# Optimization experiments

Measured on AMD Instinct MI355X. Metric: run time of the kernel, lower is better.

The kernel has to match this reference:

```python
import jax, jax.numpy as jnp
import numpy as np

B, L = 32, 512
D_EMB = 500      # tagger_mlp_layer
LANG = 100       # tagger_embeddings_size
H = 800          # tagger_encoder_size * 2
P_ARC = 100      # parser_arc_proj_size
P_LAB = 400      # parser_label_proj_size
MLP = 500        # tagger_mlp_layer (aux_mlp out)
N_LANG, N_LAB, N_UPOS, N_XPOS, N_ATTRS = 8, 50, 20, 300, 500


def setup_inputs() -> dict:
    key = jax.random.key(0)
    ks = jax.random.split(key, 24)
    s = 0.05
    lang_table = jax.random.normal(ks[3], (N_LANG, LANG), jnp.float32) * s
    lang_table = lang_table.at[0].set(0.0)  # padding_idx=0
    return {
        "emb": jax.random.normal(ks[0], (B, L, D_EMB), jnp.float32),
        "hidden": jax.random.normal(ks[1], (B, L, H), jnp.float32),
        "lang_ids": jax.random.randint(ks[2], (B,), 0, N_LANG),
        "lang_table": lang_table,
        "W_arc": jax.random.normal(ks[4], (P_ARC, D_EMB + LANG), jnp.float32) * s,
        "b_arc": jax.random.normal(ks[5], (P_ARC,), jnp.float32) * s,
        "W_lab": jax.random.normal(ks[6], (P_LAB, D_EMB + LANG), jnp.float32) * s,
        "b_lab": jax.random.normal(ks[7], (P_LAB,), jnp.float32) * s,
        "w_head": jax.random.normal(ks[8], (2 * P_ARC,), jnp.float32) * s,
        "b_head": jax.random.normal(ks[9], (1,), jnp.float32) * s,
        "W_aux": jax.random.normal(ks[10], (MLP, H), jnp.float32) * s,
        "b_aux": jax.random.normal(ks[11], (MLP,), jnp.float32) * s,
        "W_upos": jax.random.normal(ks[12], (N_UPOS, MLP + LANG), jnp.float32) * s,
        "b_upos": jax.random.normal(ks[13], (N_UPOS,), jnp.float32) * s,
        "W_xpos": jax.random.normal(ks[14], (N_XPOS, MLP + LANG), jnp.float32) * s,
        "b_xpos": jax.random.normal(ks[15], (N_XPOS,), jnp.float32) * s,
        "W_attrs": jax.random.normal(ks[16], (N_ATTRS, MLP + LANG), jnp.float32) * s,
        "b_attrs": jax.random.normal(ks[17], (N_ATTRS,), jnp.float32) * s,
    }


def reference(emb, hidden, lang_ids, lang_table, W_arc, b_arc, W_lab, b_lab,
              w_head, b_head, W_aux, b_aux, W_upos, b_upos, W_xpos, b_xpos,
              W_attrs, b_attrs):
    Bv, Lv = emb.shape[0], emb.shape[1]
    lang_emb = lang_table[lang_ids]                              # [B, LANG]
    lang_rep = jnp.broadcast_to(lang_emb[:, None, :], (Bv, Lv, lang_emb.shape[-1]))
    ho = jnp.concatenate((emb, lang_rep), axis=2)                # [B, L, D_EMB+LANG]

    proj_arc = jnp.tanh(jnp.einsum('bld,pd->blp', ho, W_arc) + b_arc)   # [B, L, P_ARC]
    proj_label = jnp.tanh(jnp.einsum('bld,pd->blp', ho, W_lab) + b_lab) # [B, L, P_LAB]

    # Biaffine decomposition of output_head(cat(pa[i], pa[j])):
    # score(i,j) = pa[i] . w1 + pa[j] . w2 + b
    P = proj_arc.shape[-1]
    s1 = proj_arc @ w_head[:P]                                   # [B, L]
    s2 = proj_arc @ w_head[P:]                                   # [B, L]
    core = s1[:, :, None] + s2[:, None, :] + b_head[0]           # [B, L, L]
    arcs = jnp.concatenate(
        (jnp.zeros((Bv, Lv, 1), core.dtype), core), axis=2)     # [B, L, L+1]

    aux_hid = jnp.tanh(jnp.einsum('blh,mh->blm', hidden, W_aux) + b_aux)  # [B, L, MLP]
    aux_cat = jnp.concatenate((aux_hid, lang_rep), axis=2)
    s_upos = jnp.einsum('blm,um->blu', aux_cat, W_upos) + b_upos
    s_xpos = jnp.einsum('blm,um->blu', aux_cat, W_xpos) + b_xpos
    s_attrs = jnp.einsum('blm,um->blu', aux_cat, W_attrs) + b_attrs
    return arcs, proj_label, s_upos, s_xpos, s_attrs
```

## Files before the change

kernel.cpp:

```cpp
#include <hip/hip_runtime.h>


using f16   = _Float16;
using f16x4 = __attribute__((ext_vector_type(4))) _Float16;
using f16x8 = __attribute__((ext_vector_type(8))) _Float16;
using f32x4 = __attribute__((ext_vector_type(4))) float;

__device__ __forceinline__ f16 f2h(float f) { return (f16)f; }
__device__ __forceinline__ f16x4 cvt4(float4 v) {
  return f16x4{ f2h(v.x), f2h(v.y), f2h(v.z), f2h(v.w) };
}

__device__ __forceinline__ float fast_tanh(float x) {
  float xc = fminf(fmaxf(x, -15.f), 15.f);
  float e  = __builtin_amdgcn_exp2f(xc * 2.885390081777927f);
  return 1.f - 2.f * __builtin_amdgcn_rcpf(e + 1.f);
}

__device__ __forceinline__ void async16(void* lds, const void* gp) {
  __builtin_amdgcn_global_load_lds(
      (const __attribute__((address_space(1))) unsigned int*)gp,
      (__attribute__((address_space(3))) unsigned int*)lds, 16, 0, 0);
}

__global__ __launch_bounds__(256) void setup_kernel(
    const float* __restrict__ W_arc, const float* __restrict__ b_arc,
    const float* __restrict__ W_lab, const float* __restrict__ b_lab,
    const float* __restrict__ W_aux, const float* __restrict__ b_aux,
    const float* __restrict__ W_upos, const float* __restrict__ b_upos,
    const float* __restrict__ W_xpos, const float* __restrict__ b_xpos,
    const float* __restrict__ W_attrs, const float* __restrict__ b_attrs,
    f16* __restrict__ W_proj, f16* __restrict__ W_auxp, f16* __restrict__ W_heads,
    float* __restrict__ bias_proj, float* __restrict__ bias_aux, float* __restrict__ bias_heads)
{
  const int blk = blockIdx.x, t = threadIdx.x;
  if (blk < 1376) {
    int w = blk * 256 + t;
    const float* src = nullptr;
    f16* dst;
    if (w < 81920) {
      int n = w / 160, s = w - n * 160;
      dst = W_proj + (size_t)w * 4;
      if (s < 150 && n < 500)
        src = (n < 100 ? W_arc + (size_t)n * 600
                       : W_lab + (size_t)(n - 100) * 600) + s * 4;
    } else if (w < 81920 + 106496) {
      int w2 = w - 81920;
      int n = w2 / 208, s = w2 - n * 208;
      dst = W_auxp + (size_t)w2 * 4;
      if (s < 200 && n < 500) src = W_aux + (size_t)n * 800 + s * 4;
    } else {
      int w3 = w - (81920 + 106496);
      int n = w3 / 160, s = w3 - n * 160;
      dst = W_heads + (size_t)w3 * 4;
      if (s < 150 && n < 820)
        src = (n < 20 ? W_upos + (size_t)n * 600
              : n < 320 ? W_xpos + (size_t)(n - 20) * 600
                        : W_attrs + (size_t)(n - 320) * 600) + s * 4;
    }
    f16x4 h = { (f16)0.f, (f16)0.f, (f16)0.f, (f16)0.f };
    if (src) h = cvt4(*(const float4*)src);
    *(f16x4*)dst = h;
    return;
  }
  for (int idx = t; idx < 2048; idx += 256) {
    if (idx < 512) {
      float v = 0.f;
      if (idx < 100)      v = b_arc[idx];
      else if (idx < 500) v = b_lab[idx - 100];
      bias_proj[idx] = v;
    } else if (idx < 1024) {
      int i = idx - 512;
      bias_aux[i] = (i < 500) ? b_aux[i] : 0.f;
    } else {
      int i = idx - 1024; float v = 0.f;
      if (i < 20)       v = b_upos[i];
      else if (i < 320) v = b_xpos[i - 20];
      else if (i < 820) v = b_attrs[i - 320];
      bias_heads[i] = v;
    }
  }
}

__global__ __launch_bounds__(512, 2) void gemm01(
    const float* __restrict__ emb, const float* __restrict__ hidden,
    const float* __restrict__ lang_table, const int* __restrict__ lang_ids,
    const f16* __restrict__ W_proj, const f16* __restrict__ W_auxp,
    const float* __restrict__ bias_proj, const float* __restrict__ bias_aux,
    float* __restrict__ out_label, const float* __restrict__ w_head,
    float* __restrict__ s1, float* __restrict__ s2, f16* __restrict__ aux_cat)
{
  __shared__ __align__(16) f16 ldsA[2 * 16384];
  __shared__ __align__(16) f16 ldsB[2 * 16384];
  __shared__ float s1red[2][256], s2red[2][256];

  const int tid  = threadIdx.x;
  const int lane = tid & 63;
  const int wave = tid >> 6;
  const int wm = wave >> 2, wn = wave & 3;
  const int m16 = lane & 15, quad = lane >> 4;
  const int bm  = blockIdx.x;
  const int bny = blockIdx.y;
  const bool is0 = (bny < 2);
  const int bn  = is0 ? bny : bny - 2;
  const int K   = is0 ? 640 : 832;
  const int NT  = is0 ? 10 : 13;

  const int sr = lane >> 3;
  const int ssB = (lane & 7) ^ sr;
  const f16* Bmat = is0 ? W_proj : W_auxp;
  const f16* gB[4];
#pragma unroll
  for (int i = 0; i < 4; ++i)
    gB[i] = Bmat + (size_t)(bn * 256 + i * 64 + wave * 8 + sr) * K + ssB * 8;
  f16* sB = ldsB + wave * 512;

  const int ssA = lane & 7;
  const float* lrow = lang_table + (size_t)lang_ids[bm >> 1] * 100;
  const float* srcA[4];
  int dstA[4];
#pragma unroll
  for (int i = 0; i < 4; ++i) {
    const int rowA = wave * 32 + i * 8 + (lane >> 3);
    const int grow = bm * 256 + rowA;
    srcA[i] = is0 ? emb + (size_t)grow * 500 : hidden + (size_t)grow * 800;
    dstA[i] = rowA * 64 + ((ssA ^ (rowA & 7)) * 8);
  }
  float4 va[4], vb[4];

  const int aBase = (wm * 128 + m16) * 64;
  const int bBase = (wn * 64  + m16) * 64;
  const int sw0 = ((quad)     ^ (m16 & 7)) * 8;
  const int sw1 = ((4 | quad) ^ (m16 & 7)) * 8;

  f32x4 acc[8][4] = {};
  f16x8 af[4], bf[4];

#define ASTAGE(tt) do { const int k0b = (tt) * 64 + ssA * 8;                    \
    _Pragma("unroll")                                                           \
    for (int i2 = 0; i2 < 4; ++i2) {                                            \
      float4 x0 = {0.f,0.f,0.f,0.f}, x1 = {0.f,0.f,0.f,0.f};                    \
      if (is0) {                                                                \
        if (k0b < 500) { x0 = *(const float4*)(srcA[i2] + k0b);                 \
          x1 = (k0b + 4 < 500) ? *(const float4*)(srcA[i2] + k0b + 4)           \
                               : *(const float4*)(lrow); }                      \
        else if (k0b < 600) { x0 = *(const float4*)(lrow + k0b - 500);          \
                              x1 = *(const float4*)(lrow + k0b - 496); }        \
      } else if (k0b < 800) { x0 = *(const float4*)(srcA[i2] + k0b);            \
                              x1 = *(const float4*)(srcA[i2] + k0b + 4); }      \
      va[i2] = x0; vb[i2] = x1; } } while (0)

#define AWRITE(nbf) do { _Pragma("unroll")                                      \
    for (int i2 = 0; i2 < 4; ++i2) {                                            \
      f16x8 hw = { f2h(va[i2].x), f2h(va[i2].y), f2h(va[i2].z), f2h(va[i2].w),  \
                   f2h(vb[i2].x), f2h(vb[i2].y), f2h(vb[i2].z), f2h(vb[i2].w) };\
      *(f16x8*)&ldsA[(nbf) + dstA[i2]] = hw; } } while (0)

#define BWISSUE(k0n, nbf) do {                                                  \
    async16(sB + (nbf) + 0 * 4096, gB[0] + (k0n));                              \
    async16(sB + (nbf) + 1 * 4096, gB[1] + (k0n));                              \
    async16(sB + (nbf) + 2 * 4096, gB[2] + (k0n));                              \
    async16(sB + (nbf) + 3 * 4096, gB[3] + (k0n)); } while (0)

#define RDA(mqv, sw) { _Pragma("unroll")                                        \
  for (int ii = 0; ii < 4; ++ii)                                                \
    af[ii] = *(const f16x8*)&ldsA[buf + aBase + (mqv) * 4096 + ii * 1024 + (sw)]; }
#define RDB(sw) { _Pragma("unroll")                                             \
  for (int j = 0; j < 4; ++j)                                                   \
    bf[j] = *(const f16x8*)&ldsB[buf + bBase + j * 1024 + (sw)]; }
#define MM(mqv) { _Pragma("unroll")                                             \
  for (int ii = 0; ii < 4; ++ii) { _Pragma("unroll")                            \
    for (int j = 0; j < 4; ++j)                                                 \
      acc[(mqv) * 4 + ii][j] = __builtin_amdgcn_mfma_f32_16x16x32_f16(          \
          af[ii], bf[j], acc[(mqv) * 4 + ii][j], 0, 0, 0); } }
#define SBAR __builtin_amdgcn_sched_barrier(0)
#define VM4  asm volatile("s_waitcnt vmcnt(4)" ::: "memory")
#define VM0  asm volatile("s_waitcnt vmcnt(0)" ::: "memory")
#define LGK0 asm volatile("s_waitcnt lgkmcnt(0)" ::: "memory")
#define BAR  __builtin_amdgcn_s_barrier()
#define PRIO1 __builtin_amdgcn_s_setprio(1)
#define PRIO0 __builtin_amdgcn_s_setprio(0)

  ASTAGE(0);
  SBAR;
  BWISSUE(0, 0);
  SBAR; VM4; SBAR;
  AWRITE(0);
  VM0;
  LGK0;
  BAR;

  for (int t = 0; t < NT; ++t) {
    const int buf = (t & 1) << 14;
    const int nbf = ((t + 1) & 1) << 14;
    const bool st = (t + 1 < NT);
    const int k0n = (t + 1) << 6;

    RDB(sw0); RDA(0, sw0);
    if (st) ASTAGE(t + 1);
    SBAR;
    if (st) BWISSUE(k0n, nbf);
    PRIO1; MM(0); PRIO0;
    RDA(1, sw0);
    PRIO1; MM(1); PRIO0;
    RDB(sw1); RDA(0, sw1);
    PRIO1; MM(0); PRIO0;
    RDA(1, sw1);
    PRIO1; MM(1); PRIO0;
    if (st) {
      SBAR; VM4; SBAR;
      AWRITE(nbf);
    }
    VM0;
    LGK0;
    BAR;
  }
#undef ASTAGE
#undef AWRITE
#undef BWISSUE
#undef RDA
#undef RDB
#undef MM
#undef SBAR
#undef VM4
#undef VM0
#undef LGK0
#undef BAR
#undef PRIO1
#undef PRIO0

  const int row0 = bm * 256 + wm * 128 + quad * 4;
  const int colT = bn * 256 + wn * 64 + m16;

  if (is0) {
    const float* bias = bias_proj;
    float p1[8][4] = {}, p2[8][4] = {};
    const bool haveHead = (bn == 0);
#pragma unroll
    for (int ai = 0; ai < 8; ++ai) {
#pragma unroll
      for (int j = 0; j < 4; ++j) {
        const int col = colT + j * 16;
        const float bcol = bias[col];
        float w1c = 0.f, w2c = 0.f;
        if (haveHead && col < 100) { w1c = w_head[col]; w2c = w_head[100 + col]; }
#pragma unroll
        for (int r = 0; r < 4; ++r) {
          const int row = row0 + ai * 16 + r;
          float v = fast_tanh(acc[ai][j][r] + bcol);
          if (col >= 100 && col < 500) out_label[(size_t)row * 400 + col - 100] = v;
          p1[ai][r] += v * w1c;
          p2[ai][r] += v * w2c;
        }
      }
    }
    if (haveHead) {
      if (wn < 2) {
#pragma unroll
        for (int d = 1; d < 16; d <<= 1)
#pragma unroll
          for (int ai = 0; ai < 8; ++ai)
#pragma unroll
            for (int r = 0; r < 4; ++r) {
              p1[ai][r] += __shfl_xor(p1[ai][r], d);
              p2[ai][r] += __shfl_xor(p2[ai][r], d);
            }
        if (m16 == 0) {
#pragma unroll
          for (int ai = 0; ai < 8; ++ai)
#pragma unroll
            for (int r = 0; r < 4; ++r) {
              int rl = wm * 128 + ai * 16 + quad * 4 + r;
              s1red[wn][rl] = p1[ai][r];
              s2red[wn][rl] = p2[ai][r];
            }
        }
      }
      __syncthreads();
      if (tid < 256) s1[bm * 256 + tid] = s1red[0][tid] + s1red[1][tid];
      else { int t2 = tid - 256; s2[bm * 256 + t2] = s2red[0][t2] + s2red[1][t2]; }
    }
  } else {
    const float* bias = bias_aux;
#pragma unroll
    for (int ai = 0; ai < 8; ++ai)
#pragma unroll
      for (int j = 0; j < 4; ++j) {
        const int col = colT + j * 16;
        if (col < 500) {
          const float bcol = bias[col];
#pragma unroll
          for (int r = 0; r < 4; ++r) {
            const int row = row0 + ai * 16 + r;
            aux_cat[(size_t)row * 640 + col] = f2h(fast_tanh(acc[ai][j][r] + bcol));
          }
        }
      }
    if (bn == 0) {
      for (int idx = tid; idx < 256 * 35; idx += 512) {
        int rr = idx / 35, qq = idx - rr * 35;
        int col = 500 + 4 * qq;
        f16x4 h = { (f16)0.f, (f16)0.f, (f16)0.f, (f16)0.f };
        if (col < 600) h = cvt4(*(const float4*)(lrow + col - 500));
        *(f16x4*)(aux_cat + (size_t)(bm * 256 + rr) * 640 + col) = h;
      }
    }
  }
}

__global__ __launch_bounds__(512, 2) void gemm2_arcs(
    const f16* __restrict__ aux_cat, const f16* __restrict__ W_heads,
    const float* __restrict__ bias_heads,
    const float* __restrict__ s1, const float* __restrict__ s2,
    const float* __restrict__ b_head,
    float* __restrict__ out_arcs, float* __restrict__ out_upos,
    float* __restrict__ out_xpos, float* __restrict__ out_attrs)
{
  __shared__ __align__(16) f16 ldsA[2 * 16384];
  __shared__ __align__(16) f16 ldsB[2 * 16384];

  const int tid  = threadIdx.x;
  const int lane = tid & 63;
  const int wave = tid >> 6;
  const int wm = wave >> 2, wn = wave & 3;
  const int m16 = lane & 15, quad = lane >> 4;
  const int bm = blockIdx.x, bn = blockIdx.y;
  const int K = 640, NT = 10;

  const int sr = lane >> 3;
  const int ss = (lane & 7) ^ sr;
  const f16* gA[4]; const f16* gB[4];
#pragma unroll
  for (int i = 0; i < 4; ++i) {
    gA[i] = aux_cat + (size_t)(bm * 256 + i * 64 + wave * 8 + sr) * K + ss * 8;
    gB[i] = W_heads + (size_t)(bn * 256 + i * 64 + wave * 8 + sr) * K + ss * 8;
  }
  f16* sA = ldsA + wave * 512;
  f16* sB = ldsB + wave * 512;

  const int aBase = (wm * 128 + m16) * 64;
  const int bBase = (wn * 64  + m16) * 64;
  const int sw0 = ((quad)     ^ (m16 & 7)) * 8;
  const int sw1 = ((4 | quad) ^ (m16 & 7)) * 8;

  f32x4 acc[8][4] = {};
  f16x8 af[4], bf[4];

#define STAGE8(k0n, nbf) do {                                                   \
    async16(sA + (nbf) + 0 * 4096, gA[0] + (k0n));                              \
    async16(sA + (nbf) + 1 * 4096, gA[1] + (k0n));                              \
    async16(sA + (nbf) + 2 * 4096, gA[2] + (k0n));                              \
    async16(sA + (nbf) + 3 * 4096, gA[3] + (k0n));                              \
    async16(sB + (nbf) + 0 * 4096, gB[0] + (k0n));                              \
    async16(sB + (nbf) + 1 * 4096, gB[1] + (k0n));                              \
    async16(sB + (nbf) + 2 * 4096, gB[2] + (k0n));                              \
    async16(sB + (nbf) + 3 * 4096, gB[3] + (k0n)); } while (0)

#define RDA(mqv, sw) { _Pragma("unroll")                                        \
  for (int ii = 0; ii < 4; ++ii)                                                \
    af[ii] = *(const f16x8*)&ldsA[buf + aBase + (mqv) * 4096 + ii * 1024 + (sw)]; }
#define RDB(sw) { _Pragma("unroll")                                             \
  for (int j = 0; j < 4; ++j)                                                   \
    bf[j] = *(const f16x8*)&ldsB[buf + bBase + j * 1024 + (sw)]; }
#define MM(mqv) { _Pragma("unroll")                                             \
  for (int ii = 0; ii < 4; ++ii) { _Pragma("unroll")                            \
    for (int j = 0; j < 4; ++j)                                                 \
      acc[(mqv) * 4 + ii][j] = __builtin_amdgcn_mfma_f32_16x16x32_f16(          \
          af[ii], bf[j], acc[(mqv) * 4 + ii][j], 0, 0, 0); } }
#define VM0  asm volatile("s_waitcnt vmcnt(0)" ::: "memory")
#define BAR  __builtin_amdgcn_s_barrier()
#define PRIO1 __builtin_amdgcn_s_setprio(1)
#define PRIO0 __builtin_amdgcn_s_setprio(0)

  STAGE8(0, 0);
  VM0;
  BAR;

  for (int t = 0; t < NT; ++t) {
    const int buf = (t & 1) << 14;
    const int nbf = ((t + 1) & 1) << 14;
    const bool st = (t + 1 < NT);
    const int k0n = (t + 1) << 6;

    RDB(sw0); RDA(0, sw0);
    if (st) STAGE8(k0n, nbf);
    PRIO1; MM(0); PRIO0;
    RDA(1, sw0);
    PRIO1; MM(1); PRIO0;
    RDB(sw1); RDA(0, sw1);
    PRIO1; MM(0); PRIO0;
    RDA(1, sw1);
    PRIO1; MM(1); PRIO0;
    VM0;
    BAR;
  }
#undef STAGE8
#undef RDA
#undef RDB
#undef MM
#undef VM0
#undef BAR
#undef PRIO1
#undef PRIO0

  const int row0 = bm * 256 + wm * 128 + quad * 4;
  const int colT = bn * 256 + wn * 64 + m16;
#pragma unroll
  for (int ai = 0; ai < 8; ++ai)
#pragma unroll
    for (int j = 0; j < 4; ++j) {
      const int col = colT + j * 16;
      const float bcol = bias_heads[col];
#pragma unroll
      for (int r = 0; r < 4; ++r) {
        const int row = row0 + ai * 16 + r;
        float v = acc[ai][j][r] + bcol;
        if (col < 20)        out_upos[(size_t)row * 20 + col] = v;
        else if (col < 320)  out_xpos[(size_t)row * 300 + col - 20] = v;
        else if (col < 820)  out_attrs[(size_t)row * 500 + col - 320] = v;
      }
    }

  const int r0 = bm * 256 + bn * 64;
  const float bh = b_head[0];
  const float s2v = s2[((r0 >> 9) << 9) + tid];
  for (int rl = 0; rl < 64; ++rl) {
    const int row = r0 + rl;
    const float s1v = s1[row] + bh;
    float* orow = out_arcs + (size_t)row * 513;
    if (tid == 0) orow[0] = 0.f;
    orow[1 + tid] = s1v + s2v;
  }
}

extern "C" void kernel_launch(void* const* d_in, const int* in_sizes, int n_in,
                              void* d_out, int out_size, void* d_ws, size_t ws_size,
                              hipStream_t stream)
{
  const float* emb      = (const float*)d_in[0];
  const float* hidden   = (const float*)d_in[1];
  const int*   lang_ids = (const int*)d_in[2];
  const float* lang_tab = (const float*)d_in[3];
  const float* W_arc  = (const float*)d_in[4];
  const float* b_arc  = (const float*)d_in[5];
  const float* W_lab  = (const float*)d_in[6];
  const float* b_lab  = (const float*)d_in[7];
  const float* w_head = (const float*)d_in[8];
  const float* b_head = (const float*)d_in[9];
  const float* W_aux  = (const float*)d_in[10];
  const float* b_aux  = (const float*)d_in[11];
  const float* W_upos = (const float*)d_in[12];
  const float* b_upos = (const float*)d_in[13];
  const float* W_xpos = (const float*)d_in[14];
  const float* b_xpos = (const float*)d_in[15];
  const float* W_attrs = (const float*)d_in[16];
  const float* b_attrs = (const float*)d_in[17];

  char* ws = (char*)d_ws;
  f16* aux_cat = (f16*)(ws + 0);
  f16* W_proj  = (f16*)(ws + 20971520);
  f16* W_auxp  = (f16*)(ws + 21626880);
  f16* W_heads = (f16*)(ws + 22478848);
  float* bias_proj  = (float*)(ws + 23789568);
  float* bias_aux   = (float*)(ws + 23791616);
  float* bias_heads = (float*)(ws + 23793664);
  float* s1         = (float*)(ws + 23797760);
  float* s2         = (float*)(ws + 23863296);

  float* out       = (float*)d_out;
  float* out_arcs  = out;
  float* out_label = out + 8404992;
  float* out_upos  = out + 14958592;
  float* out_xpos  = out + 15286272;
  float* out_attrs = out + 20201472;

  setup_kernel<<<1377, 256, 0, stream>>>(
      W_arc, b_arc, W_lab, b_lab, W_aux, b_aux,
      W_upos, b_upos, W_xpos, b_xpos, W_attrs, b_attrs,
      W_proj, W_auxp, W_heads, bias_proj, bias_aux, bias_heads);

  gemm01<<<dim3(64, 4), 512, 0, stream>>>(
      emb, hidden, lang_tab, lang_ids, W_proj, W_auxp, bias_proj, bias_aux,
      out_label, w_head, s1, s2, aux_cat);

  gemm2_arcs<<<dim3(64, 4), 512, 0, stream>>>(
      aux_cat, W_heads, bias_heads, s1, s2, b_head,
      out_arcs, out_upos, out_xpos, out_attrs);
}
```

Before: 267.2 us.

## Shrink GEMM tiles to 128x128x32 with 256-thread blocks and triple-buffered A

Both GEMM kernels move from 256x256 tiles with K-step 64 and 512 threads to 128x128 tiles with K-step 32 and 256 threads. This gives four times as many blocks (1024 instead of 256) to fill the 256 CUs, and uses a new LDS swizzle. The aux weight matrix is no longer padded to K=832, which drops the padded K iterations. gemm2 gains a three-stage A pipeline, and the arcs write is re-split across rows. In exchange, each block reuses less data, so more of A and B must be read from L2, and there are more barriers per unit of work.

```diff
diff --git a/kernel.cpp b/kernel.cpp
--- a/kernel.cpp
+++ b/kernel.cpp
@@ -34,7 +34,7 @@
     float* __restrict__ bias_proj, float* __restrict__ bias_aux, float* __restrict__ bias_heads)
 {
   const int blk = blockIdx.x, t = threadIdx.x;
-  if (blk < 1376) {
+  if (blk < 1360) {
     int w = blk * 256 + t;
     const float* src = nullptr;
     f16* dst;
@@ -44,13 +44,12 @@
       if (s < 150 && n < 500)
         src = (n < 100 ? W_arc + (size_t)n * 600
                        : W_lab + (size_t)(n - 100) * 600) + s * 4;
-    } else if (w < 81920 + 106496) {
+    } else if (w < 184320) {
       int w2 = w - 81920;
-      int n = w2 / 208, s = w2 - n * 208;
       dst = W_auxp + (size_t)w2 * 4;
-      if (s < 200 && n < 500) src = W_aux + (size_t)n * 800 + s * 4;
+      if (w2 < 100000) src = W_aux + (size_t)w2 * 4;
     } else {
-      int w3 = w - (81920 + 106496);
+      int w3 = w - 184320;
       int n = w3 / 160, s = w3 - n * 160;
       dst = W_heads + (size_t)w3 * 4;
       if (s < 150 && n < 820)
@@ -82,7 +81,7 @@
   }
 }
 
-__global__ __launch_bounds__(512, 2) void gemm01(
+__global__ __launch_bounds__(256, 4) void gemm01(
     const float* __restrict__ emb, const float* __restrict__ hidden,
     const float* __restrict__ lang_table, const int* __restrict__ lang_ids,
     const f16* __restrict__ W_proj, const f16* __restrict__ W_auxp,
@@ -90,55 +89,55 @@
     float* __restrict__ out_label, const float* __restrict__ w_head,
     float* __restrict__ s1, float* __restrict__ s2, f16* __restrict__ aux_cat)
 {
-  __shared__ __align__(16) f16 ldsA[2 * 16384];
-  __shared__ __align__(16) f16 ldsB[2 * 16384];
-  __shared__ float s1red[2][256], s2red[2][256];
+  __shared__ __align__(16) f16 ldsA[2 * 4096];
+  __shared__ __align__(16) f16 ldsB[2 * 4096];
+  __shared__ float s1red[2][128], s2red[2][128];
 
   const int tid  = threadIdx.x;
   const int lane = tid & 63;
   const int wave = tid >> 6;
-  const int wm = wave >> 2, wn = wave & 3;
+  const int wm = wave >> 1, wn = wave & 1;
   const int m16 = lane & 15, quad = lane >> 4;
   const int bm  = blockIdx.x;
   const int bny = blockIdx.y;
-  const bool is0 = (bny < 2);
-  const int bn  = is0 ? bny : bny - 2;
-  const int K   = is0 ? 640 : 832;
-  const int NT  = is0 ? 10 : 13;
-
-  const int sr = lane >> 3;
-  const int ssB = (lane & 7) ^ sr;
+  const bool is0 = (bny < 4);
+  const int bn  = is0 ? bny : bny - 4;
+  const int K   = is0 ? 640 : 800;
+  const int NT  = is0 ? 20 : 25;
+
+  const int sigR  = (m16 & 3) ^ ((m16 >> 2) & 3);
+  const int sigS  = ((lane >> 2) & 3) ^ quad;
+  const int kap   = lane & 3;
+
   const f16* Bmat = is0 ? W_proj : W_auxp;
-  const f16* gB[4];
-#pragma unroll
-  for (int i = 0; i < 4; ++i)
-    gB[i] = Bmat + (size_t)(bn * 256 + i * 64 + wave * 8 + sr) * K + ssB * 8;
-  f16* sB = ldsB + wave * 512;
-
-  const int ssA = lane & 7;
-  const float* lrow = lang_table + (size_t)lang_ids[bm >> 1] * 100;
-  const float* srcA[4];
-  int dstA[4];
-#pragma unroll
-  for (int i = 0; i < 4; ++i) {
-    const int rowA = wave * 32 + i * 8 + (lane >> 3);
-    const int grow = bm * 256 + rowA;
+  const int kapB = kap ^ sigS;
+  const f16* gB[2];
+#pragma unroll
+  for (int j = 0; j < 2; ++j)
+    gB[j] = Bmat + (size_t)(bn * 128 + wave * 32 + j * 16 + (lane >> 2)) * K + kapB * 8;
+  const int sBoff = wave * 1024;
+
+  const float* lrow = lang_table + (size_t)lang_ids[bm >> 2] * 100;
+  const float* srcA[2];
+  int dstA[2];
+#pragma unroll
+  for (int i = 0; i < 2; ++i) {
+    const int rowL = wave * 32 + i * 16 + (lane >> 2);
+    const int grow = bm * 128 + rowL;
     srcA[i] = is0 ? emb + (size_t)grow * 500 : hidden + (size_t)grow * 800;
-    dstA[i] = rowA * 64 + ((ssA ^ (rowA & 7)) * 8);
-  }
-  float4 va[4], vb[4];
-
-  const int aBase = (wm * 128 + m16) * 64;
-  const int bBase = (wn * 64  + m16) * 64;
-  const int sw0 = ((quad)     ^ (m16 & 7)) * 8;
-  const int sw1 = ((4 | quad) ^ (m16 & 7)) * 8;
-
-  f32x4 acc[8][4] = {};
+    dstA[i] = rowL * 32 + ((kap ^ sigS) * 8);
+  }
+  float4 va[2], vb[2];
+
+  const int baseA = (wm * 64 + m16) * 32 + ((quad ^ sigR) * 8);
+  const int baseB = (wn * 64 + m16) * 32 + ((quad ^ sigR) * 8);
+
+  f32x4 acc[4][4] = {};
   f16x8 af[4], bf[4];
 
-#define ASTAGE(tt) do { const int k0b = (tt) * 64 + ssA * 8;                    \
+#define ASTAGE(tt) do { const int k0b = (tt) * 32 + kap * 8;                    \
     _Pragma("unroll")                                                           \
-    for (int i2 = 0; i2 < 4; ++i2) {                                            \
+    for (int i2 = 0; i2 < 2; ++i2) {                                            \
       float4 x0 = {0.f,0.f,0.f,0.f}, x1 = {0.f,0.f,0.f,0.f};                    \
       if (is0) {                                                                \
         if (k0b < 500) { x0 = *(const float4*)(srcA[i2] + k0b);                 \
@@ -146,35 +145,33 @@
                                : *(const float4*)(lrow); }                      \
         else if (k0b < 600) { x0 = *(const float4*)(lrow + k0b - 500);          \
                               x1 = *(const float4*)(lrow + k0b - 496); }        \
-      } else if (k0b < 800) { x0 = *(const float4*)(srcA[i2] + k0b);            \
-                              x1 = *(const float4*)(srcA[i2] + k0b + 4); }      \
+      } else { x0 = *(const float4*)(srcA[i2] + k0b);                           \
+               x1 = *(const float4*)(srcA[i2] + k0b + 4); }                     \
       va[i2] = x0; vb[i2] = x1; } } while (0)
 
-#define AWRITE(nbf) do { _Pragma("unroll")                                      \
-    for (int i2 = 0; i2 < 4; ++i2) {                                            \
+#define AWRITE(nbfA) do { _Pragma("unroll")                                     \
+    for (int i2 = 0; i2 < 2; ++i2) {                                            \
       f16x8 hw = { f2h(va[i2].x), f2h(va[i2].y), f2h(va[i2].z), f2h(va[i2].w),  \
                    f2h(vb[i2].x), f2h(vb[i2].y), f2h(vb[i2].z), f2h(vb[i2].w) };\
-      *(f16x8*)&ldsA[(nbf) + dstA[i2]] = hw; } } while (0)
-
-#define BWISSUE(k0n, nbf) do {                                                  \
-    async16(sB + (nbf) + 0 * 4096, gB[0] + (k0n));                              \
-    async16(sB + (nbf) + 1 * 4096, gB[1] + (k0n));                              \
-    async16(sB + (nbf) + 2 * 4096, gB[2] + (k0n));                              \
-    async16(sB + (nbf) + 3 * 4096, gB[3] + (k0n)); } while (0)
-
-#define RDA(mqv, sw) { _Pragma("unroll")                                        \
+      *(f16x8*)&ldsA[(nbfA) + dstA[i2]] = hw; } } while (0)
+
+#define BWISSUE(tt, nbfB) do {                                                  \
+    async16(&ldsB[(nbfB) + sBoff],       gB[0] + (tt) * 32);                    \
+    async16(&ldsB[(nbfB) + sBoff + 512], gB[1] + (tt) * 32); } while (0)
+
+#define RD8(bA, bB) { _Pragma("unroll")                                         \
   for (int ii = 0; ii < 4; ++ii)                                                \
-    af[ii] = *(const f16x8*)&ldsA[buf + aBase + (mqv) * 4096 + ii * 1024 + (sw)]; }
-#define RDB(sw) { _Pragma("unroll")                                             \
+    af[ii] = *(const f16x8*)&ldsA[(bA) + baseA + ii * 512];                     \
+  _Pragma("unroll")                                                             \
   for (int j = 0; j < 4; ++j)                                                   \
-    bf[j] = *(const f16x8*)&ldsB[buf + bBase + j * 1024 + (sw)]; }
-#define MM(mqv) { _Pragma("unroll")                                             \
+    bf[j] = *(const f16x8*)&ldsB[(bB) + baseB + j * 512]; }
+#define MM { _Pragma("unroll")                                                  \
   for (int ii = 0; ii < 4; ++ii) { _Pragma("unroll")                            \
     for (int j = 0; j < 4; ++j)                                                 \
-      acc[(mqv) * 4 + ii][j] = __builtin_amdgcn_mfma_f32_16x16x32_f16(          \
-          af[ii], bf[j], acc[(mqv) * 4 + ii][j], 0, 0, 0); } }
+      acc[ii][j] = __builtin_amdgcn_mfma_f32_16x16x32_f16(                      \
+          af[ii], bf[j], acc[ii][j], 0, 0, 0); } }
 #define SBAR __builtin_amdgcn_sched_barrier(0)
-#define VM4  asm volatile("s_waitcnt vmcnt(4)" ::: "memory")
+#define VM2  asm volatile("s_waitcnt vmcnt(2)" ::: "memory")
 #define VM0  asm volatile("s_waitcnt vmcnt(0)" ::: "memory")
 #define LGK0 asm volatile("s_waitcnt lgkmcnt(0)" ::: "memory")
 #define BAR  __builtin_amdgcn_s_barrier()
@@ -184,64 +181,56 @@
   ASTAGE(0);
   SBAR;
   BWISSUE(0, 0);
-  SBAR; VM4; SBAR;
+  SBAR; VM2; SBAR;
   AWRITE(0);
   VM0;
   LGK0;
   BAR;
 
+  int bufA = 0, bufB = 0;
   for (int t = 0; t < NT; ++t) {
-    const int buf = (t & 1) << 14;
-    const int nbf = ((t + 1) & 1) << 14;
     const bool st = (t + 1 < NT);
-    const int k0n = (t + 1) << 6;
-
-    RDB(sw0); RDA(0, sw0);
+    const int nA = bufA ^ 4096, nB = bufB ^ 4096;
+
     if (st) ASTAGE(t + 1);
     SBAR;
-    if (st) BWISSUE(k0n, nbf);
-    PRIO1; MM(0); PRIO0;
-    RDA(1, sw0);
-    PRIO1; MM(1); PRIO0;
-    RDB(sw1); RDA(0, sw1);
-    PRIO1; MM(0); PRIO0;
-    RDA(1, sw1);
-    PRIO1; MM(1); PRIO0;
+    if (st) BWISSUE(t + 1, nB);
+    RD8(bufA, bufB);
+    PRIO1; MM; PRIO0;
     if (st) {
-      SBAR; VM4; SBAR;
-      AWRITE(nbf);
+      SBAR; VM2; SBAR;
+      AWRITE(nA);
     }
     VM0;
     LGK0;
     BAR;
+    bufA = nA; bufB = nB;
   }
 #undef ASTAGE
 #undef AWRITE
 #undef BWISSUE
-#undef RDA
-#undef RDB
+#undef RD8
 #undef MM
 #undef SBAR
-#undef VM4
+#undef VM2
 #undef VM0
 #undef LGK0
 #undef BAR
 #undef PRIO1
 #undef PRIO0
 
-  const int row0 = bm * 256 + wm * 128 + quad * 4;
-  const int colT = bn * 256 + wn * 64 + m16;
+  const int row0 = bm * 128 + wm * 64 + quad * 4;
+  const int colT = bn * 128 + wn * 64 + m16;
 
   if (is0) {
-    const float* bias = bias_proj;
-    float p1[8][4] = {}, p2[8][4] = {};
     const bool haveHead = (bn == 0);
 #pragma unroll
-    for (int ai = 0; ai < 8; ++ai) {
+    for (int ai = 0; ai < 4; ++ai) {
+      float p1r[4] = {}, p2r[4] = {};
 #pragma unroll
       for (int j = 0; j < 4; ++j) {
         const int col = colT + j * 16;
-        const float bcol = bias[col];
+        const float bcol = bias_proj[col];
         float w1c = 0.f, w2c = 0.f;
         if (haveHead && col < 100) { w1c = w_head[col]; w2c = w_head[100 + col]; }
 #pragma unroll
@@ -249,46 +238,41 @@
           const int row = row0 + ai * 16 + r;
           float v = fast_tanh(acc[ai][j][r] + bcol);
           if (col >= 100 && col < 500) out_label[(size_t)row * 400 + col - 100] = v;
-          p1[ai][r] += v * w1c;
-          p2[ai][r] += v * w2c;
+          p1r[r] += v * w1c;
+          p2r[r] += v * w2c;
         }
       }
-    }
-    if (haveHead) {
-      if (wn < 2) {
+      if (haveHead) {
 #pragma unroll
         for (int d = 1; d < 16; d <<= 1)
 #pragma unroll
-          for (int ai = 0; ai < 8; ++ai)
-#pragma unroll
-            for (int r = 0; r < 4; ++r) {
-              p1[ai][r] += __shfl_xor(p1[ai][r], d);
-              p2[ai][r] += __shfl_xor(p2[ai][r], d);
-            }
+          for (int r = 0; r < 4; ++r) {
+            p1r[r] += __shfl_xor(p1r[r], d);
+            p2r[r] += __shfl_xor(p2r[r], d);
+          }
         if (m16 == 0) {
 #pragma unroll
-          for (int ai = 0; ai < 8; ++ai)
-#pragma unroll
-            for (int r = 0; r < 4; ++r) {
-              int rl = wm * 128 + ai * 16 + quad * 4 + r;
-              s1red[wn][rl] = p1[ai][r];
-              s2red[wn][rl] = p2[ai][r];
-            }
+          for (int r = 0; r < 4; ++r) {
+            int rl = wm * 64 + ai * 16 + quad * 4 + r;
+            s1red[wn][rl] = p1r[r];
+            s2red[wn][rl] = p2r[r];
+          }
         }
       }
+    }
+    if (haveHead) {
       __syncthreads();
-      if (tid < 256) s1[bm * 256 + tid] = s1red[0][tid] + s1red[1][tid];
-      else { int t2 = tid - 256; s2[bm * 256 + t2] = s2red[0][t2] + s2red[1][t2]; }
+      if (tid < 128)       s1[bm * 128 + tid] = s1red[0][tid] + s1red[1][tid];
+      else                 s2[bm * 128 + tid - 128] = s2red[0][tid - 128] + s2red[1][tid - 128];
     }
   } else {
-    const float* bias = bias_aux;
-#pragma unroll
-    for (int ai = 0; ai < 8; ++ai)
+#pragma unroll
+    for (int ai = 0; ai < 4; ++ai)
 #pragma unroll
       for (int j = 0; j < 4; ++j) {
         const int col = colT + j * 16;
         if (col < 500) {
-          const float bcol = bias[col];
+          const float bcol = bias_aux[col];
 #pragma unroll
           for (int r = 0; r < 4; ++r) {
             const int row = row0 + ai * 16 + r;
@@ -297,18 +281,18 @@
         }
       }
     if (bn == 0) {
-      for (int idx = tid; idx < 256 * 35; idx += 512) {
+      for (int idx = tid; idx < 128 * 35; idx += 256) {
         int rr = idx / 35, qq = idx - rr * 35;
         int col = 500 + 4 * qq;
         f16x4 h = { (f16)0.f, (f16)0.f, (f16)0.f, (f16)0.f };
         if (col < 600) h = cvt4(*(const float4*)(lrow + col - 500));
-        *(f16x4*)(aux_cat + (size_t)(bm * 256 + rr) * 640 + col) = h;
+        *(f16x4*)(aux_cat + (size_t)(bm * 128 + rr) * 640 + col) = h;
       }
     }
   }
 }
 
-__global__ __launch_bounds__(512, 2) void gemm2_arcs(
+__global__ __launch_bounds__(256, 4) void gemm2_arcs(
     const f16* __restrict__ aux_cat, const f16* __restrict__ W_heads,
     const float* __restrict__ bias_heads,
     const float* __restrict__ s1, const float* __restrict__ s2,
@@ -316,97 +300,97 @@
     float* __restrict__ out_arcs, float* __restrict__ out_upos,
     float* __restrict__ out_xpos, float* __restrict__ out_attrs)
 {
-  __shared__ __align__(16) f16 ldsA[2 * 16384];
-  __shared__ __align__(16) f16 ldsB[2 * 16384];
+  __shared__ __align__(16) f16 ldsA[3 * 4096];
+  __shared__ __align__(16) f16 ldsB[2 * 4096];
 
   const int tid  = threadIdx.x;
   const int lane = tid & 63;
   const int wave = tid >> 6;
-  const int wm = wave >> 2, wn = wave & 3;
+  const int wm = wave >> 1, wn = wave & 1;
   const int m16 = lane & 15, quad = lane >> 4;
   const int bm = blockIdx.x, bn = blockIdx.y;
-  const int K = 640, NT = 10;
-
-  const int sr = lane >> 3;
-  const int ss = (lane & 7) ^ sr;
-  const f16* gA[4]; const f16* gB[4];
-#pragma unroll
-  for (int i = 0; i < 4; ++i) {
-    gA[i] = aux_cat + (size_t)(bm * 256 + i * 64 + wave * 8 + sr) * K + ss * 8;
-    gB[i] = W_heads + (size_t)(bn * 256 + i * 64 + wave * 8 + sr) * K + ss * 8;
-  }
-  f16* sA = ldsA + wave * 512;
-  f16* sB = ldsB + wave * 512;
-
-  const int aBase = (wm * 128 + m16) * 64;
-  const int bBase = (wn * 64  + m16) * 64;
-  const int sw0 = ((quad)     ^ (m16 & 7)) * 8;
-  const int sw1 = ((4 | quad) ^ (m16 & 7)) * 8;
-
-  f32x4 acc[8][4] = {};
+  const int NT = 20;
+
+  const int sigR = (m16 & 3) ^ ((m16 >> 2) & 3);
+  const int sigS = ((lane >> 2) & 3) ^ quad;
+  const int kapS = (lane & 3) ^ sigS;
+
+  const f16* gA[2]; const f16* gB[2];
+#pragma unroll
+  for (int j = 0; j < 2; ++j) {
+    const int rsub = wave * 32 + j * 16 + (lane >> 2);
+    gA[j] = aux_cat + (size_t)(bm * 128 + rsub) * 640 + kapS * 8;
+    gB[j] = W_heads + (size_t)(bn * 128 + rsub) * 640 + kapS * 8;
+  }
+  const int sOff = wave * 1024;
+
+  const int baseA = (wm * 64 + m16) * 32 + ((quad ^ sigR) * 8);
+  const int baseB = (wn * 64 + m16) * 32 + ((quad ^ sigR) * 8);
+
+  f32x4 acc[4][4] = {};
   f16x8 af[4], bf[4];
 
-#define STAGE8(k0n, nbf) do {                                                   \
-    async16(sA + (nbf) + 0 * 4096, gA[0] + (k0n));                              \
-    async16(sA + (nbf) + 1 * 4096, gA[1] + (k0n));                              \
-    async16(sA + (nbf) + 2 * 4096, gA[2] + (k0n));                              \
-    async16(sA + (nbf) + 3 * 4096, gA[3] + (k0n));                              \
-    async16(sB + (nbf) + 0 * 4096, gB[0] + (k0n));                              \
-    async16(sB + (nbf) + 1 * 4096, gB[1] + (k0n));                              \
-    async16(sB + (nbf) + 2 * 4096, gB[2] + (k0n));                              \
-    async16(sB + (nbf) + 3 * 4096, gB[3] + (k0n)); } while (0)
-
-#define RDA(mqv, sw) { _Pragma("unroll")                                        \
+#define SA(tt, bA) do {                                                         \
+    async16(&ldsA[(bA) + sOff],       gA[0] + (tt) * 32);                       \
+    async16(&ldsA[(bA) + sOff + 512], gA[1] + (tt) * 32); } while (0)
+#define SB(tt, bB) do {                                                         \
+    async16(&ldsB[(bB) + sOff],       gB[0] + (tt) * 32);                       \
+    async16(&ldsB[(bB) + sOff + 512], gB[1] + (tt) * 32); } while (0)
+#define RD8(bA, bB) { _Pragma("unroll")                                         \
   for (int ii = 0; ii < 4; ++ii)                                                \
-    af[ii] = *(const f16x8*)&ldsA[buf + aBase + (mqv) * 4096 + ii * 1024 + (sw)]; }
-#define RDB(sw) { _Pragma("unroll")                                             \
+    af[ii] = *(const f16x8*)&ldsA[(bA) + baseA + ii * 512];                     \
+  _Pragma("unroll")                                                             \
   for (int j = 0; j < 4; ++j)                                                   \
-    bf[j] = *(const f16x8*)&ldsB[buf + bBase + j * 1024 + (sw)]; }
-#define MM(mqv) { _Pragma("unroll")                                             \
+    bf[j] = *(const f16x8*)&ldsB[(bB) + baseB + j * 512]; }
+#define MM { _Pragma("unroll")                                                  \
   for (int ii = 0; ii < 4; ++ii) { _Pragma("unroll")                            \
     for (int j = 0; j < 4; ++j)                                                 \
-      acc[(mqv) * 4 + ii][j] = __builtin_amdgcn_mfma_f32_16x16x32_f16(          \
-          af[ii], bf[j], acc[(mqv) * 4 + ii][j], 0, 0, 0); } }
+      acc[ii][j] = __builtin_amdgcn_mfma_f32_16x16x32_f16(                      \
+          af[ii], bf[j], acc[ii][j], 0, 0, 0); } }
+#define SBAR __builtin_amdgcn_sched_barrier(0)
+#define VM2  asm volatile("s_waitcnt vmcnt(2)" ::: "memory")
 #define VM0  asm volatile("s_waitcnt vmcnt(0)" ::: "memory")
 #define BAR  __builtin_amdgcn_s_barrier()
 #define PRIO1 __builtin_amdgcn_s_setprio(1)
 #define PRIO0 __builtin_amdgcn_s_setprio(0)
 
-  STAGE8(0, 0);
-  VM0;
+  SA(0, 0);
+  SBAR;
+  SB(0, 0);
+  SBAR;
+  SA(1, 4096);
+  VM2;
   BAR;
 
+  int a0 = 0, a1 = 4096, a2 = 8192, b0 = 0;
   for (int t = 0; t < NT; ++t) {
-    const int buf = (t & 1) << 14;
-    const int nbf = ((t + 1) & 1) << 14;
-    const bool st = (t + 1 < NT);
-    const int k0n = (t + 1) << 6;
-
-    RDB(sw0); RDA(0, sw0);
-    if (st) STAGE8(k0n, nbf);
-    PRIO1; MM(0); PRIO0;
-    RDA(1, sw0);
-    PRIO1; MM(1); PRIO0;
-    RDB(sw1); RDA(0, sw1);
-    PRIO1; MM(0); PRIO0;
-    RDA(1, sw1);
-    PRIO1; MM(1); PRIO0;
-    VM0;
+    const bool st1 = (t + 1 < NT), st2 = (t + 2 < NT);
+
+    if (st1) SB(t + 1, b0 ^ 4096);
+    SBAR;
+    if (st2) SA(t + 2, a2);
+    RD8(a0, b0);
+    PRIO1; MM; PRIO0;
+    if (st2) VM2; else VM0;
     BAR;
-  }
-#undef STAGE8
-#undef RDA
-#undef RDB
+    int rot = a0; a0 = a1; a1 = a2; a2 = rot;
+    b0 ^= 4096;
+  }
+#undef SA
+#undef SB
+#undef RD8
 #undef MM
+#undef SBAR
+#undef VM2
 #undef VM0
 #undef BAR
 #undef PRIO1
 #undef PRIO0
 
-  const int row0 = bm * 256 + wm * 128 + quad * 4;
-  const int colT = bn * 256 + wn * 64 + m16;
-#pragma unroll
-  for (int ai = 0; ai < 8; ++ai)
+  const int row0 = bm * 128 + wm * 64 + quad * 4;
+  const int colT = bn * 128 + wn * 64 + m16;
+#pragma unroll
+  for (int ai = 0; ai < 4; ++ai)
 #pragma unroll
     for (int j = 0; j < 4; ++j) {
       const int col = colT + j * 16;
@@ -421,15 +405,19 @@
       }
     }
 
-  const int r0 = bm * 256 + bn * 64;
+  const int r0 = bm * 128 + bn * 16;
+  const int b = bm >> 2;
   const float bh = b_head[0];
-  const float s2v = s2[((r0 >> 9) << 9) + tid];
-  for (int rl = 0; rl < 64; ++rl) {
+  const float s2a = s2[(b << 9) + tid];
+  const float s2b = s2[(b << 9) + 256 + tid];
+#pragma unroll
+  for (int rl = 0; rl < 16; ++rl) {
     const int row = r0 + rl;
     const float s1v = s1[row] + bh;
     float* orow = out_arcs + (size_t)row * 513;
     if (tid == 0) orow[0] = 0.f;
-    orow[1 + tid] = s1v + s2v;
+    orow[1 + tid] = s1v + s2a;
+    orow[257 + tid] = s1v + s2b;
   }
 }
 
@@ -460,12 +448,12 @@
   f16* aux_cat = (f16*)(ws + 0);
   f16* W_proj  = (f16*)(ws + 20971520);
   f16* W_auxp  = (f16*)(ws + 21626880);
-  f16* W_heads = (f16*)(ws + 22478848);
-  float* bias_proj  = (float*)(ws + 23789568);
-  float* bias_aux   = (float*)(ws + 23791616);
-  float* bias_heads = (float*)(ws + 23793664);
-  float* s1         = (float*)(ws + 23797760);
-  float* s2         = (float*)(ws + 23863296);
+  f16* W_heads = (f16*)(ws + 22446080);
+  float* bias_proj  = (float*)(ws + 23756800);
+  float* bias_aux   = (float*)(ws + 23758848);
+  float* bias_heads = (float*)(ws + 23760896);
+  float* s1         = (float*)(ws + 23764992);
+  float* s2         = (float*)(ws + 23830528);
 
   float* out       = (float*)d_out;
   float* out_arcs  = out;
@@ -474,16 +462,16 @@
   float* out_xpos  = out + 15286272;
   float* out_attrs = out + 20201472;
 
-  setup_kernel<<<1377, 256, 0, stream>>>(
+  setup_kernel<<<1361, 256, 0, stream>>>(
       W_arc, b_arc, W_lab, b_lab, W_aux, b_aux,
       W_upos, b_upos, W_xpos, b_xpos, W_attrs, b_attrs,
       W_proj, W_auxp, W_heads, bias_proj, bias_aux, bias_heads);
 
-  gemm01<<<dim3(64, 4), 512, 0, stream>>>(
+  gemm01<<<dim3(128, 8), 256, 0, stream>>>(
       emb, hidden, lang_tab, lang_ids, W_proj, W_auxp, bias_proj, bias_aux,
       out_label, w_head, s1, s2, aux_cat);
 
-  gemm2_arcs<<<dim3(64, 4), 512, 0, stream>>>(
+  gemm2_arcs<<<dim3(128, 8), 256, 0, stream>>>(
       aux_cat, W_heads, bias_heads, s1, s2, b_head,
       out_arcs, out_upos, out_xpos, out_attrs);
 }
```

After: 312.7 us. +17.0%, slower.

## Deepen async prefetch to three-stage LDS buffering in both GEMM kernels

Applied to the files above, without the earlier changes.

In gemm01 the weight (B) tiles are now triple-buffered and prefetched two K-steps ahead, while A stays double-buffered through registers. LDS is a single 160KB raw array aliased for the head-reduction scratch. In the heads GEMM the A tiles are triple-buffered and prefetched two steps ahead with partial vmcnt waits, so a load no longer has to drain fully at every iteration. The aim is to hide global-load latency behind MFMA work. The cost is much more LDS per block, which can cut occupancy below the declared two blocks per CU.

```diff
diff --git a/kernel.cpp b/kernel.cpp
--- a/kernel.cpp
+++ b/kernel.cpp
@@ -90,9 +90,11 @@
     float* __restrict__ out_label, const float* __restrict__ w_head,
     float* __restrict__ s1, float* __restrict__ s2, f16* __restrict__ aux_cat)
 {
-  __shared__ __align__(16) f16 ldsA[2 * 16384];
-  __shared__ __align__(16) f16 ldsB[2 * 16384];
-  __shared__ float s1red[2][256], s2red[2][256];
+  __shared__ __align__(16) char smem[163840];
+  f16* ldsA = (f16*)smem;
+  f16* ldsB = (f16*)(smem + 65536);
+  float* s1redp = (float*)smem;
+  float* s2redp = (float*)(smem + 2048);
 
   const int tid  = threadIdx.x;
   const int lane = tid & 63;
@@ -150,30 +152,31 @@
                               x1 = *(const float4*)(srcA[i2] + k0b + 4); }      \
       va[i2] = x0; vb[i2] = x1; } } while (0)
 
-#define AWRITE(nbf) do { _Pragma("unroll")                                      \
+#define AWRITE(nbfA) do { _Pragma("unroll")                                     \
     for (int i2 = 0; i2 < 4; ++i2) {                                            \
       f16x8 hw = { f2h(va[i2].x), f2h(va[i2].y), f2h(va[i2].z), f2h(va[i2].w),  \
                    f2h(vb[i2].x), f2h(vb[i2].y), f2h(vb[i2].z), f2h(vb[i2].w) };\
-      *(f16x8*)&ldsA[(nbf) + dstA[i2]] = hw; } } while (0)
-
-#define BWISSUE(k0n, nbf) do {                                                  \
-    async16(sB + (nbf) + 0 * 4096, gB[0] + (k0n));                              \
-    async16(sB + (nbf) + 1 * 4096, gB[1] + (k0n));                              \
-    async16(sB + (nbf) + 2 * 4096, gB[2] + (k0n));                              \
-    async16(sB + (nbf) + 3 * 4096, gB[3] + (k0n)); } while (0)
-
-#define RDA(mqv, sw) { _Pragma("unroll")                                        \
+      *(f16x8*)&ldsA[(nbfA) + dstA[i2]] = hw; } } while (0)
+
+#define BWISSUE(tt, bBuf) do { const int k0w = (tt) << 6;                       \
+    async16(sB + (bBuf) + 0 * 4096, gB[0] + k0w);                               \
+    async16(sB + (bBuf) + 1 * 4096, gB[1] + k0w);                               \
+    async16(sB + (bBuf) + 2 * 4096, gB[2] + k0w);                               \
+    async16(sB + (bBuf) + 3 * 4096, gB[3] + k0w); } while (0)
+
+#define RDA(mqv, sw, bA) { _Pragma("unroll")                                    \
   for (int ii = 0; ii < 4; ++ii)                                                \
-    af[ii] = *(const f16x8*)&ldsA[buf + aBase + (mqv) * 4096 + ii * 1024 + (sw)]; }
-#define RDB(sw) { _Pragma("unroll")                                             \
+    af[ii] = *(const f16x8*)&ldsA[(bA) + aBase + (mqv) * 4096 + ii * 1024 + (sw)]; }
+#define RDB(sw, bB) { _Pragma("unroll")                                         \
   for (int j = 0; j < 4; ++j)                                                   \
-    bf[j] = *(const f16x8*)&ldsB[buf + bBase + j * 1024 + (sw)]; }
+    bf[j] = *(const f16x8*)&ldsB[(bB) + bBase + j * 1024 + (sw)]; }
 #define MM(mqv) { _Pragma("unroll")                                             \
   for (int ii = 0; ii < 4; ++ii) { _Pragma("unroll")                            \
     for (int j = 0; j < 4; ++j)                                                 \
       acc[(mqv) * 4 + ii][j] = __builtin_amdgcn_mfma_f32_16x16x32_f16(          \
           af[ii], bf[j], acc[(mqv) * 4 + ii][j], 0, 0, 0); } }
 #define SBAR __builtin_amdgcn_sched_barrier(0)
+#define VM8  asm volatile("s_waitcnt vmcnt(8)" ::: "memory")
 #define VM4  asm volatile("s_waitcnt vmcnt(4)" ::: "memory")
 #define VM0  asm volatile("s_waitcnt vmcnt(0)" ::: "memory")
 #define LGK0 asm volatile("s_waitcnt lgkmcnt(0)" ::: "memory")
@@ -184,36 +187,40 @@
   ASTAGE(0);
   SBAR;
   BWISSUE(0, 0);
-  SBAR; VM4; SBAR;
+  BWISSUE(1, 16384);
+  SBAR; VM8; SBAR;
   AWRITE(0);
-  VM0;
+  VM4;
   LGK0;
   BAR;
 
+  int bufA = 0;
+  int bB0 = 0, bB1 = 16384, bB2 = 32768;
   for (int t = 0; t < NT; ++t) {
-    const int buf = (t & 1) << 14;
-    const int nbf = ((t + 1) & 1) << 14;
-    const bool st = (t + 1 < NT);
-    const int k0n = (t + 1) << 6;
-
-    RDB(sw0); RDA(0, sw0);
-    if (st) ASTAGE(t + 1);
+    const int nA = bufA ^ 16384;
+    const bool st1 = (t + 1 < NT), st2 = (t + 2 < NT);
+
+    if (st1) ASTAGE(t + 1);
     SBAR;
-    if (st) BWISSUE(k0n, nbf);
+    if (st2) BWISSUE(t + 2, bB2);
+    RDB(sw0, bB0); RDA(0, sw0, bufA);
     PRIO1; MM(0); PRIO0;
-    RDA(1, sw0);
+    RDA(1, sw0, bufA);
     PRIO1; MM(1); PRIO0;
-    RDB(sw1); RDA(0, sw1);
+    RDB(sw1, bB0); RDA(0, sw1, bufA);
     PRIO1; MM(0); PRIO0;
-    RDA(1, sw1);
+    RDA(1, sw1, bufA);
     PRIO1; MM(1); PRIO0;
-    if (st) {
-      SBAR; VM4; SBAR;
-      AWRITE(nbf);
-    }
-    VM0;
+    if (st1) {
+      SBAR;
+      if (st2) VM4; else VM0;
+      SBAR;
+      AWRITE(nA);
+    }
     LGK0;
     BAR;
+    bufA = nA;
+    int tmp = bB0; bB0 = bB1; bB1 = bB2; bB2 = tmp;
   }
 #undef ASTAGE
 #undef AWRITE
@@ -222,6 +229,7 @@
 #undef RDB
 #undef MM
 #undef SBAR
+#undef VM8
 #undef VM4
 #undef VM0
 #undef LGK0
@@ -271,14 +279,14 @@
 #pragma unroll
             for (int r = 0; r < 4; ++r) {
               int rl = wm * 128 + ai * 16 + quad * 4 + r;
-              s1red[wn][rl] = p1[ai][r];
-              s2red[wn][rl] = p2[ai][r];
+              s1redp[wn * 256 + rl] = p1[ai][r];
+              s2redp[wn * 256 + rl] = p2[ai][r];
             }
         }
       }
       __syncthreads();
-      if (tid < 256) s1[bm * 256 + tid] = s1red[0][tid] + s1red[1][tid];
-      else { int t2 = tid - 256; s2[bm * 256 + t2] = s2red[0][t2] + s2red[1][t2]; }
+      if (tid < 256) s1[bm * 256 + tid] = s1redp[tid] + s1redp[256 + tid];
+      else { int t2 = tid - 256; s2[bm * 256 + t2] = s2redp[t2] + s2redp[256 + t2]; }
     }
   } else {
     const float* bias = bias_aux;
@@ -316,7 +324,7 @@
     float* __restrict__ out_arcs, float* __restrict__ out_upos,
     float* __restrict__ out_xpos, float* __restrict__ out_attrs)
 {
-  __shared__ __align__(16) f16 ldsA[2 * 16384];
+  __shared__ __align__(16) f16 ldsA[3 * 16384];
   __shared__ __align__(16) f16 ldsB[2 * 16384];
 
   const int tid  = threadIdx.x;
@@ -346,58 +354,69 @@
   f32x4 acc[8][4] = {};
   f16x8 af[4], bf[4];
 
-#define STAGE8(k0n, nbf) do {                                                   \
-    async16(sA + (nbf) + 0 * 4096, gA[0] + (k0n));                              \
-    async16(sA + (nbf) + 1 * 4096, gA[1] + (k0n));                              \
-    async16(sA + (nbf) + 2 * 4096, gA[2] + (k0n));                              \
-    async16(sA + (nbf) + 3 * 4096, gA[3] + (k0n));                              \
-    async16(sB + (nbf) + 0 * 4096, gB[0] + (k0n));                              \
-    async16(sB + (nbf) + 1 * 4096, gB[1] + (k0n));                              \
-    async16(sB + (nbf) + 2 * 4096, gB[2] + (k0n));                              \
-    async16(sB + (nbf) + 3 * 4096, gB[3] + (k0n)); } while (0)
-
-#define RDA(mqv, sw) { _Pragma("unroll")                                        \
+#define SA4(tt, bA) do { const int k0w = (tt) << 6;                             \
+    async16(sA + (bA) + 0 * 4096, gA[0] + k0w);                                 \
+    async16(sA + (bA) + 1 * 4096, gA[1] + k0w);                                 \
+    async16(sA + (bA) + 2 * 4096, gA[2] + k0w);                                 \
+    async16(sA + (bA) + 3 * 4096, gA[3] + k0w); } while (0)
+#define SB4(tt, bB) do { const int k0w = (tt) << 6;                             \
+    async16(sB + (bB) + 0 * 4096, gB[0] + k0w);                                 \
+    async16(sB + (bB) + 1 * 4096, gB[1] + k0w);                                 \
+    async16(sB + (bB) + 2 * 4096, gB[2] + k0w);                                 \
+    async16(sB + (bB) + 3 * 4096, gB[3] + k0w); } while (0)
+#define RDA(mqv, sw, bA) { _Pragma("unroll")                                    \
   for (int ii = 0; ii < 4; ++ii)                                                \
-    af[ii] = *(const f16x8*)&ldsA[buf + aBase + (mqv) * 4096 + ii * 1024 + (sw)]; }
-#define RDB(sw) { _Pragma("unroll")                                             \
+    af[ii] = *(const f16x8*)&ldsA[(bA) + aBase + (mqv) * 4096 + ii * 1024 + (sw)]; }
+#define RDB(sw, bB) { _Pragma("unroll")                                         \
   for (int j = 0; j < 4; ++j)                                                   \
-    bf[j] = *(const f16x8*)&ldsB[buf + bBase + j * 1024 + (sw)]; }
+    bf[j] = *(const f16x8*)&ldsB[(bB) + bBase + j * 1024 + (sw)]; }
 #define MM(mqv) { _Pragma("unroll")                                             \
   for (int ii = 0; ii < 4; ++ii) { _Pragma("unroll")                            \
     for (int j = 0; j < 4; ++j)                                                 \
       acc[(mqv) * 4 + ii][j] = __builtin_amdgcn_mfma_f32_16x16x32_f16(          \
           af[ii], bf[j], acc[(mqv) * 4 + ii][j], 0, 0, 0); } }
+#define SBAR __builtin_amdgcn_sched_barrier(0)
+#define VM4  asm volatile("s_waitcnt vmcnt(4)" ::: "memory")
 #define VM0  asm volatile("s_waitcnt vmcnt(0)" ::: "memory")
 #define BAR  __builtin_amdgcn_s_barrier()
 #define PRIO1 __builtin_amdgcn_s_setprio(1)
 #define PRIO0 __builtin_amdgcn_s_setprio(0)
 
-  STAGE8(0, 0);
-  VM0;
+  SA4(0, 0);
+  SBAR;
+  SB4(0, 0);
+  SBAR;
+  SA4(1, 16384);
+  VM4;
   BAR;
 
+  int a0 = 0, a1 = 16384, a2 = 32768, b0 = 0;
   for (int t = 0; t < NT; ++t) {
-    const int buf = (t & 1) << 14;
-    const int nbf = ((t + 1) & 1) << 14;
-    const bool st = (t + 1 < NT);
-    const int k0n = (t + 1) << 6;
-
-    RDB(sw0); RDA(0, sw0);
-    if (st) STAGE8(k0n, nbf);
+    const bool st1 = (t + 1 < NT), st2 = (t + 2 < NT);
+
+    if (st1) SB4(t + 1, b0 ^ 16384);
+    SBAR;
+    if (st2) SA4(t + 2, a2);
+    RDB(sw0, b0); RDA(0, sw0, a0);
     PRIO1; MM(0); PRIO0;
-    RDA(1, sw0);
+    RDA(1, sw0, a0);
     PRIO1; MM(1); PRIO0;
-    RDB(sw1); RDA(0, sw1);
+    RDB(sw1, b0); RDA(0, sw1, a0);
     PRIO1; MM(0); PRIO0;
-    RDA(1, sw1);
+    RDA(1, sw1, a0);
     PRIO1; MM(1); PRIO0;
-    VM0;
+    if (st2) VM4; else VM0;
     BAR;
-  }
-#undef STAGE8
+    int rot = a0; a0 = a1; a1 = a2; a2 = rot;
+    b0 ^= 16384;
+  }
+#undef SA4
+#undef SB4
 #undef RDA
 #undef RDB
 #undef MM
+#undef SBAR
+#undef VM4
 #undef VM0
 #undef BAR
 #undef PRIO1
```

Result: slower. 280.1 us (+4.8%).

## Triple-buffer A tiles in gemm2 to prefetch two k-steps ahead

Applied to the files above, without the earlier changes.

The head GEMM main loop moves from a double-buffered A/B pipeline to a triple-buffered A with double-buffered B. A tiles are prefetched two iterations ahead and the loop waits only with vmcnt(4), so one stage of loads stays in flight across the barrier. This aims to hide global-to-LDS latency better, at the cost of 32KB more LDS, which may reduce occupancy below the launch-bounds target of two blocks per CU.

```diff
diff --git a/kernel.cpp b/kernel.cpp
--- a/kernel.cpp
+++ b/kernel.cpp
@@ -316,7 +316,7 @@
     float* __restrict__ out_arcs, float* __restrict__ out_upos,
     float* __restrict__ out_xpos, float* __restrict__ out_attrs)
 {
-  __shared__ __align__(16) f16 ldsA[2 * 16384];
+  __shared__ __align__(16) f16 ldsA[3 * 16384];
   __shared__ __align__(16) f16 ldsB[2 * 16384];
 
   const int tid  = threadIdx.x;
@@ -346,58 +346,69 @@
   f32x4 acc[8][4] = {};
   f16x8 af[4], bf[4];
 
-#define STAGE8(k0n, nbf) do {                                                   \
-    async16(sA + (nbf) + 0 * 4096, gA[0] + (k0n));                              \
-    async16(sA + (nbf) + 1 * 4096, gA[1] + (k0n));                              \
-    async16(sA + (nbf) + 2 * 4096, gA[2] + (k0n));                              \
-    async16(sA + (nbf) + 3 * 4096, gA[3] + (k0n));                              \
-    async16(sB + (nbf) + 0 * 4096, gB[0] + (k0n));                              \
-    async16(sB + (nbf) + 1 * 4096, gB[1] + (k0n));                              \
-    async16(sB + (nbf) + 2 * 4096, gB[2] + (k0n));                              \
-    async16(sB + (nbf) + 3 * 4096, gB[3] + (k0n)); } while (0)
-
-#define RDA(mqv, sw) { _Pragma("unroll")                                        \
+#define SA4(tt, bA) do { const int k0w = (tt) << 6;                             \
+    async16(sA + (bA) + 0 * 4096, gA[0] + k0w);                                 \
+    async16(sA + (bA) + 1 * 4096, gA[1] + k0w);                                 \
+    async16(sA + (bA) + 2 * 4096, gA[2] + k0w);                                 \
+    async16(sA + (bA) + 3 * 4096, gA[3] + k0w); } while (0)
+#define SB4(tt, bB) do { const int k0w = (tt) << 6;                             \
+    async16(sB + (bB) + 0 * 4096, gB[0] + k0w);                                 \
+    async16(sB + (bB) + 1 * 4096, gB[1] + k0w);                                 \
+    async16(sB + (bB) + 2 * 4096, gB[2] + k0w);                                 \
+    async16(sB + (bB) + 3 * 4096, gB[3] + k0w); } while (0)
+#define RDA(mqv, sw, bA) { _Pragma("unroll")                                    \
   for (int ii = 0; ii < 4; ++ii)                                                \
-    af[ii] = *(const f16x8*)&ldsA[buf + aBase + (mqv) * 4096 + ii * 1024 + (sw)]; }
-#define RDB(sw) { _Pragma("unroll")                                             \
+    af[ii] = *(const f16x8*)&ldsA[(bA) + aBase + (mqv) * 4096 + ii * 1024 + (sw)]; }
+#define RDB(sw, bB) { _Pragma("unroll")                                         \
   for (int j = 0; j < 4; ++j)                                                   \
-    bf[j] = *(const f16x8*)&ldsB[buf + bBase + j * 1024 + (sw)]; }
+    bf[j] = *(const f16x8*)&ldsB[(bB) + bBase + j * 1024 + (sw)]; }
 #define MM(mqv) { _Pragma("unroll")                                             \
   for (int ii = 0; ii < 4; ++ii) { _Pragma("unroll")                            \
     for (int j = 0; j < 4; ++j)                                                 \
       acc[(mqv) * 4 + ii][j] = __builtin_amdgcn_mfma_f32_16x16x32_f16(          \
           af[ii], bf[j], acc[(mqv) * 4 + ii][j], 0, 0, 0); } }
+#define SBAR __builtin_amdgcn_sched_barrier(0)
+#define VM4  asm volatile("s_waitcnt vmcnt(4)" ::: "memory")
 #define VM0  asm volatile("s_waitcnt vmcnt(0)" ::: "memory")
 #define BAR  __builtin_amdgcn_s_barrier()
 #define PRIO1 __builtin_amdgcn_s_setprio(1)
 #define PRIO0 __builtin_amdgcn_s_setprio(0)
 
-  STAGE8(0, 0);
-  VM0;
+  SA4(0, 0);
+  SBAR;
+  SB4(0, 0);
+  SBAR;
+  SA4(1, 16384);
+  VM4;
   BAR;
 
+  int a0 = 0, a1 = 16384, a2 = 32768, b0 = 0;
   for (int t = 0; t < NT; ++t) {
-    const int buf = (t & 1) << 14;
-    const int nbf = ((t + 1) & 1) << 14;
-    const bool st = (t + 1 < NT);
-    const int k0n = (t + 1) << 6;
-
-    RDB(sw0); RDA(0, sw0);
-    if (st) STAGE8(k0n, nbf);
+    const bool st1 = (t + 1 < NT), st2 = (t + 2 < NT);
+
+    if (st1) SB4(t + 1, b0 ^ 16384);
+    SBAR;
+    if (st2) SA4(t + 2, a2);
+    RDB(sw0, b0); RDA(0, sw0, a0);
     PRIO1; MM(0); PRIO0;
-    RDA(1, sw0);
+    RDA(1, sw0, a0);
     PRIO1; MM(1); PRIO0;
-    RDB(sw1); RDA(0, sw1);
+    RDB(sw1, b0); RDA(0, sw1, a0);
     PRIO1; MM(0); PRIO0;
-    RDA(1, sw1);
+    RDA(1, sw1, a0);
     PRIO1; MM(1); PRIO0;
-    VM0;
+    if (st2) VM4; else VM0;
     BAR;
-  }
-#undef STAGE8
+    int rot = a0; a0 = a1; a1 = a2; a2 = rot;
+    b0 ^= 16384;
+  }
+#undef SA4
+#undef SB4
 #undef RDA
 #undef RDB
 #undef MM
+#undef SBAR
+#undef VM4
 #undef VM0
 #undef BAR
 #undef PRIO1
```

Measured after the change: 270.2 us. No clear change (+1.1%).
